# Performance work log

Measured on AMD Instinct MI355X. Metric: run time of the kernel, lower is better.

## Reference

```python
import jax, jax.numpy as jnp
import numpy as np

K = 32          # num_sets (experts)
D_IN = 10       # input_size
D_H = 20        # hidden_size
D_OUT = 1       # output_size
B = 262144      # batch


def setup_inputs() -> dict:
    key = jax.random.key(0)
    ks = jax.random.split(key, 6)
    # Kaiming-uniform-ish init scale like torch Linear defaults
    s1 = 1.0 / np.sqrt(D_IN)
    s2 = 1.0 / np.sqrt(D_H)
    return {
        "input_data": jax.random.normal(ks[0], (B, D_IN), dtype=jnp.float32),
        "W1": jax.random.uniform(ks[1], (K, D_H, D_IN), jnp.float32, -s1, s1),
        "b1": jax.random.uniform(ks[2], (K, D_H), jnp.float32, -s1, s1),
        "W2": jax.random.uniform(ks[3], (K, D_OUT, D_H), jnp.float32, -s2, s2),
        "b2": jax.random.uniform(ks[4], (K, D_OUT), jnp.float32, -s2, s2),
        "prototypes": jax.random.normal(ks[5], (K, D_IN), dtype=jnp.float32),
    }


def reference(input_data, W1, b1, W2, b2, prototypes):
    # All K tiny experts as one batched GEMM: [B,K,H]
    h = jax.nn.relu(jnp.einsum("bi,khi->bkh", input_data, W1) + b1[None])
    preds = jnp.einsum("bkh,koh->bko", h, W2) + b2[None]          # [B,K,O]
    # Distance-based softmax gating over experts
    diff = input_data[:, None, :] - prototypes[None, :, :]        # [B,K,D]
    dist = jnp.sqrt(jnp.sum(diff * diff, axis=2))                 # [B,K]
    attn = jax.nn.softmax(-dist, axis=1)                          # [B,K]
    return jnp.sum(preds * attn[:, :, None], axis=1)              # [B,O]
```

## Files before the change

### kernel.cpp

```cpp
#include <hip/hip_runtime.h>


#define KX 32
#define DIN 10
#define DH 20
#define BLOCK 512
#define WPB 8
#define TPW 2

typedef short bf16x8 __attribute__((ext_vector_type(8)));
typedef float f32x16 __attribute__((ext_vector_type(16)));
typedef float v2f    __attribute__((ext_vector_type(2)));

#define ZERO16 {0.f,0.f,0.f,0.f, 0.f,0.f,0.f,0.f, 0.f,0.f,0.f,0.f, 0.f,0.f,0.f,0.f}

__device__ inline unsigned short f2bf(float f) {
    unsigned int u = __float_as_uint(f);
    unsigned int r = u + 0x7fffu + ((u >> 16) & 1u);
    return (unsigned short)(r >> 16);
}

union BFU { bf16x8 v; unsigned short s[8]; };

__global__ __launch_bounds__(BLOCK, 4) void moe_kernel(
    const float* __restrict__ x,
    const float* __restrict__ W1,
    const float* __restrict__ b1,
    const float* __restrict__ W2,
    const float* __restrict__ b2,
    const float* __restrict__ proto,
    float* __restrict__ out,
    int B)
{
    __shared__ bf16x8 s_af[KX * 40];
    __shared__ float  s_w2[KX * 24];
    __shared__ bf16x8 s_pf[64];
    __shared__ float  s_pn2[32];
    __shared__ float  s_b2c[32];

    const int tid = threadIdx.x;

    for (int idx = tid; idx < KX * 40; idx += BLOCK) {
        const int e = idx / 40, rem = idx - e * 40;
        const int ks = rem / 20, h = rem - ks * 20;
        BFU u;
#pragma unroll
        for (int j = 0; j < 8; ++j) {
            const int kk = ks * 8 + j;
            float v = 0.f;
            if (kk < DIN) v = W1[(e * DH + h) * DIN + kk];
            else if (kk == DIN) v = b1[e * DH + h];
            u.s[j] = f2bf(v);
        }
        s_af[idx] = u.v;
    }
    for (int idx = tid; idx < KX * 24; idx += BLOCK) {
        const int e = idx / 24, rem = idx - e * 24;
        const int hf = rem / 12, q = rem - hf * 12;
        float v = 0.f;
        if (q < 10) {
            const int m = (q & 3) + 8 * (q >> 2) + 4 * hf;
            const int h = (m & 3) + 4 * (m >> 3) + ((m & 4) ? 10 : 0);
            v = W2[e * DH + h];
        }
        s_w2[idx] = v;
    }
    if (tid < 64) {
        const int m = tid & 31, kb = (tid >> 5) * 8;
        BFU u;
#pragma unroll
        for (int j = 0; j < 8; ++j) {
            const int kk = kb + j;
            u.s[j] = f2bf(kk < DIN ? proto[m * DIN + kk] : 0.f);
        }
        s_pf[tid] = u.v;
    }
    if (tid < 32) {
        const int hf = tid >> 4, q = tid & 15;
        const int p = (q & 3) + 8 * (q >> 2) + 4 * hf;
        float s = 0.f;
#pragma unroll
        for (int i = 0; i < DIN; ++i) { const float v = proto[p * DIN + i]; s = fmaf(v, v, s); }
        s_pn2[tid] = s;
        s_b2c[tid] = b2[p];
    }
    __syncthreads();

    const int lane = tid & 63;
    const int wave = tid >> 6;
    const int half = lane >> 5;
    const int col  = lane & 31;
    const bf16x8 pfrag = s_pf[lane];

    const f32x16 kZero = ZERO16;

    const int m = col;
    const bool mvalid = (m & 4) ? (m < 22) : (m < 18);
    const int hidx = (m & 3) + 4 * (m >> 3) + ((m & 4) ? 10 : 0);
    const int abase = half * 20 + (mvalid ? hidx : 0);

#pragma unroll 1
    for (int t = 0; t < TPW; ++t) {
        const int row = ((blockIdx.x * WPB + wave) * TPW + t) * 32 + col;
        const int rr = (row < B) ? row : (B - 1);

        float xe[8];
        const float* xr = x + (size_t)rr * DIN;
        if (half == 0) {
#pragma unroll
            for (int i = 0; i < 4; ++i) {
                const float2 v = *(const float2*)(xr + 2 * i);
                xe[2 * i] = v.x; xe[2 * i + 1] = v.y;
            }
        } else {
            const float2 v = *(const float2*)(xr + 8);
            xe[0] = v.x; xe[1] = v.y; xe[2] = 1.f;
            xe[3] = 0.f; xe[4] = 0.f; xe[5] = 0.f; xe[6] = 0.f; xe[7] = 0.f;
        }
        BFU xu;
#pragma unroll
        for (int j = 0; j < 8; ++j) xu.s[j] = f2bf(xe[j]);
        const bf16x8 xfrag = xu.v;

        float part;
        if (half == 0) {
            part = 0.f;
#pragma unroll
            for (int j = 0; j < 8; ++j) part = fmaf(xe[j], xe[j], part);
        } else {
            part = fmaf(xe[0], xe[0], xe[1] * xe[1]);
        }
        const float xn2 = part + __shfl_xor(part, 32);

        const f32x16 dotg = __builtin_amdgcn_mfma_f32_32x32x16_bf16(pfrag, xfrag, kZero, 0, 0, 0);

        float gate[16], gx[16];
        float dsum = 0.f;
        float nsA = 0.f, nsB = 0.f;
        {
            const float* pn2h = s_pn2 + half * 16;
            const float* b2c  = s_b2c + half * 16;
#pragma unroll
            for (int q = 0; q < 16; ++q) {
                float d2 = fmaf(dotg[q], -2.f, xn2 + pn2h[q]);
                d2 = fmaxf(d2, 0.f);
                const float g = __expf(-__fsqrt_rn(d2));
                gate[q] = g;
                dsum += g;
                nsA = fmaf(g, b2c[q], nsA);
            }
#pragma unroll
            for (int q = 0; q < 16; ++q) gx[q] = __shfl_xor(gate[q], 32);
        }

#pragma unroll 2
        for (int j = 0; j < 16; ++j) {
            const int elo = (j & 3) + 8 * (j >> 2);
            const int ehi = elo + 4;

            bf16x8 alo = {0, 0, 0, 0, 0, 0, 0, 0};
            bf16x8 ahi = {0, 0, 0, 0, 0, 0, 0, 0};
            if (mvalid) {
                alo = s_af[elo * 40 + abase];
                ahi = s_af[ehi * 40 + abase];
            }
            const f32x16 clo = __builtin_amdgcn_mfma_f32_32x32x16_bf16(alo, xfrag, kZero, 0, 0, 0);
            const f32x16 chi = __builtin_amdgcn_mfma_f32_32x32x16_bf16(ahi, xfrag, kZero, 0, 0, 0);

            const float4* w4lo = (const float4*)(s_w2 + elo * 24 + half * 12);
            const float4* w4hi = (const float4*)(s_w2 + ehi * 24 + half * 12);
            v2f plov = v2f{0.f, 0.f}, phiv = v2f{0.f, 0.f};
#pragma unroll
            for (int i = 0; i < 3; ++i) {
                const float4 wl = w4lo[i];
                const float4 wh = w4hi[i];
                v2f cl0 = __builtin_elementwise_max(v2f{clo[4 * i + 0], clo[4 * i + 1]}, v2f{0.f, 0.f});
                v2f cl1 = __builtin_elementwise_max(v2f{clo[4 * i + 2], clo[4 * i + 3]}, v2f{0.f, 0.f});
                v2f ch0 = __builtin_elementwise_max(v2f{chi[4 * i + 0], chi[4 * i + 1]}, v2f{0.f, 0.f});
                v2f ch1 = __builtin_elementwise_max(v2f{chi[4 * i + 2], chi[4 * i + 3]}, v2f{0.f, 0.f});
                plov = __builtin_elementwise_fma(cl0, v2f{wl.x, wl.y}, plov);
                plov = __builtin_elementwise_fma(cl1, v2f{wl.z, wl.w}, plov);
                phiv = __builtin_elementwise_fma(ch0, v2f{wh.x, wh.y}, phiv);
                phiv = __builtin_elementwise_fma(ch1, v2f{wh.z, wh.w}, phiv);
            }
            const float pplo = plov.x + plov.y;
            const float pphi = phiv.x + phiv.y;

            const float p_own = half ? pphi : pplo;
            const float p_oth = half ? pplo : pphi;
            nsA = fmaf(gate[j], p_own, nsA);
            nsB = fmaf(gx[j],   p_oth, nsB);
        }

        float nsum = nsA + nsB;
        nsum += __shfl_xor(nsum, 32);
        dsum += __shfl_xor(dsum, 32);
        if (half == 0 && row < B) out[row] = nsum / dsum;
    }
}

extern "C" void kernel_launch(void* const* d_in, const int* in_sizes, int n_in,
                              void* d_out, int out_size, void* d_ws, size_t ws_size,
                              hipStream_t stream) {
    const float* x     = (const float*)d_in[0];
    const float* W1    = (const float*)d_in[1];
    const float* b1    = (const float*)d_in[2];
    const float* W2    = (const float*)d_in[3];
    const float* b2    = (const float*)d_in[4];
    const float* proto = (const float*)d_in[5];
    float* out = (float*)d_out;

    const int B = out_size;
    const int rows_per_block = WPB * TPW * 32;
    const int grid = (B + rows_per_block - 1) / rows_per_block;
    hipLaunchKernelGGL(moe_kernel, dim3(grid), dim3(BLOCK), 0, stream,
                       x, W1, b1, W2, b2, proto, out, B);
}
```

Baseline: 96.74 us.

## Interchange tile and expert loops to reuse W1/W2 fragments across row tiles

The loop order changes so both row tiles per wave are processed inside the expert loop. Each expert's A-fragment and W2 LDS reads are now loaded once and reused for both tiles, which cuts LDS traffic. The gate shuffle is replaced by shuffling the partial predictions, and b2 is read straight from global memory instead of staged through shared memory. The cost is higher register pressure from holding the gates for both tiles, plus more cross-lane shuffles per expert.

```diff
diff --git a/kernel.cpp b/kernel.cpp
--- a/kernel.cpp
+++ b/kernel.cpp
@@ -36,7 +36,6 @@
     __shared__ float  s_w2[KX * 24];
     __shared__ bf16x8 s_pf[64];
     __shared__ float  s_pn2[32];
-    __shared__ float  s_b2c[32];
 
     const int tid = threadIdx.x;
 
@@ -82,7 +81,6 @@
 #pragma unroll
         for (int i = 0; i < DIN; ++i) { const float v = proto[p * DIN + i]; s = fmaf(v, v, s); }
         s_pn2[tid] = s;
-        s_b2c[tid] = b2[p];
     }
     __syncthreads();
 
@@ -91,7 +89,6 @@
     const int half = lane >> 5;
     const int col  = lane & 31;
     const bf16x8 pfrag = s_pf[lane];
-
     const f32x16 kZero = ZERO16;
 
     const int m = col;
@@ -99,10 +96,15 @@
     const int hidx = (m & 3) + 4 * (m >> 3) + ((m & 4) ? 10 : 0);
     const int abase = half * 20 + (mvalid ? hidx : 0);
 
-#pragma unroll 1
+    int   row[TPW];
+    bf16x8 xfrag[TPW];
+    float gate[TPW][16];
+    float nsum[TPW], dsum[TPW];
+
+#pragma unroll
     for (int t = 0; t < TPW; ++t) {
-        const int row = ((blockIdx.x * WPB + wave) * TPW + t) * 32 + col;
-        const int rr = (row < B) ? row : (B - 1);
+        row[t] = ((blockIdx.x * WPB + wave) * TPW + t) * 32 + col;
+        const int rr = (row[t] < B) ? row[t] : (B - 1);
 
         float xe[8];
         const float* xr = x + (size_t)rr * DIN;
@@ -120,7 +122,7 @@
         BFU xu;
 #pragma unroll
         for (int j = 0; j < 8; ++j) xu.s[j] = f2bf(xe[j]);
-        const bf16x8 xfrag = xu.v;
+        xfrag[t] = xu.v;
 
         float part;
         if (half == 0) {
@@ -132,70 +134,85 @@
         }
         const float xn2 = part + __shfl_xor(part, 32);
 
-        const f32x16 dotg = __builtin_amdgcn_mfma_f32_32x32x16_bf16(pfrag, xfrag, kZero, 0, 0, 0);
-
-        float gate[16], gx[16];
-        float dsum = 0.f;
-        float nsA = 0.f, nsB = 0.f;
-        {
-            const float* pn2h = s_pn2 + half * 16;
-            const float* b2c  = s_b2c + half * 16;
-#pragma unroll
-            for (int q = 0; q < 16; ++q) {
-                float d2 = fmaf(dotg[q], -2.f, xn2 + pn2h[q]);
-                d2 = fmaxf(d2, 0.f);
-                const float g = __expf(-__fsqrt_rn(d2));
-                gate[q] = g;
-                dsum += g;
-                nsA = fmaf(g, b2c[q], nsA);
-            }
-#pragma unroll
-            for (int q = 0; q < 16; ++q) gx[q] = __shfl_xor(gate[q], 32);
-        }
+        const f32x16 dotg = __builtin_amdgcn_mfma_f32_32x32x16_bf16(pfrag, xfrag[t], kZero, 0, 0, 0);
+        const float* pn2h = s_pn2 + half * 16;
+        float ds = 0.f;
+#pragma unroll
+        for (int q = 0; q < 16; ++q) {
+            float d2 = fmaf(dotg[q], -2.f, xn2 + pn2h[q]);
+            d2 = fmaxf(d2, 0.f);
+            const float g = __expf(-__fsqrt_rn(d2));
+            gate[t][q] = g;
+            ds += g;
+        }
+        dsum[t] = ds;
+        nsum[t] = 0.f;
+    }
 
 #pragma unroll 2
-        for (int j = 0; j < 16; ++j) {
-            const int elo = (j & 3) + 8 * (j >> 2);
-            const int ehi = elo + 4;
-
-            bf16x8 alo = {0, 0, 0, 0, 0, 0, 0, 0};
-            bf16x8 ahi = {0, 0, 0, 0, 0, 0, 0, 0};
-            if (mvalid) {
-                alo = s_af[elo * 40 + abase];
-                ahi = s_af[ehi * 40 + abase];
-            }
-            const f32x16 clo = __builtin_amdgcn_mfma_f32_32x32x16_bf16(alo, xfrag, kZero, 0, 0, 0);
-            const f32x16 chi = __builtin_amdgcn_mfma_f32_32x32x16_bf16(ahi, xfrag, kZero, 0, 0, 0);
-
-            const float4* w4lo = (const float4*)(s_w2 + elo * 24 + half * 12);
-            const float4* w4hi = (const float4*)(s_w2 + ehi * 24 + half * 12);
+    for (int j = 0; j < 16; ++j) {
+        const int elo = (j & 3) + 8 * (j >> 2);
+        const int ehi = elo + 4;
+
+        bf16x8 alo = {0, 0, 0, 0, 0, 0, 0, 0};
+        bf16x8 ahi = {0, 0, 0, 0, 0, 0, 0, 0};
+        if (mvalid) {
+            alo = s_af[elo * 40 + abase];
+            ahi = s_af[ehi * 40 + abase];
+        }
+        const float4* w4lo = (const float4*)(s_w2 + elo * 24 + half * 12);
+        const float4* w4hi = (const float4*)(s_w2 + ehi * 24 + half * 12);
+        const float4 wl0 = w4lo[0], wl1 = w4lo[1], wl2 = w4lo[2];
+        const float4 wh0 = w4hi[0], wh1 = w4hi[1], wh2 = w4hi[2];
+
+#pragma unroll
+        for (int t = 0; t < TPW; ++t) {
+            const f32x16 clo = __builtin_amdgcn_mfma_f32_32x32x16_bf16(alo, xfrag[t], kZero, 0, 0, 0);
+            const f32x16 chi = __builtin_amdgcn_mfma_f32_32x32x16_bf16(ahi, xfrag[t], kZero, 0, 0, 0);
+
             v2f plov = v2f{0.f, 0.f}, phiv = v2f{0.f, 0.f};
-#pragma unroll
-            for (int i = 0; i < 3; ++i) {
-                const float4 wl = w4lo[i];
-                const float4 wh = w4hi[i];
-                v2f cl0 = __builtin_elementwise_max(v2f{clo[4 * i + 0], clo[4 * i + 1]}, v2f{0.f, 0.f});
-                v2f cl1 = __builtin_elementwise_max(v2f{clo[4 * i + 2], clo[4 * i + 3]}, v2f{0.f, 0.f});
-                v2f ch0 = __builtin_elementwise_max(v2f{chi[4 * i + 0], chi[4 * i + 1]}, v2f{0.f, 0.f});
-                v2f ch1 = __builtin_elementwise_max(v2f{chi[4 * i + 2], chi[4 * i + 3]}, v2f{0.f, 0.f});
-                plov = __builtin_elementwise_fma(cl0, v2f{wl.x, wl.y}, plov);
-                plov = __builtin_elementwise_fma(cl1, v2f{wl.z, wl.w}, plov);
-                phiv = __builtin_elementwise_fma(ch0, v2f{wh.x, wh.y}, phiv);
-                phiv = __builtin_elementwise_fma(ch1, v2f{wh.z, wh.w}, phiv);
+            {
+                v2f c;
+                c = __builtin_elementwise_max(v2f{clo[0],  clo[1]},  v2f{0.f, 0.f});
+                plov = __builtin_elementwise_fma(c, v2f{wl0.x, wl0.y}, plov);
+                c = __builtin_elementwise_max(v2f{clo[2],  clo[3]},  v2f{0.f, 0.f});
+                plov = __builtin_elementwise_fma(c, v2f{wl0.z, wl0.w}, plov);
+                c = __builtin_elementwise_max(v2f{clo[4],  clo[5]},  v2f{0.f, 0.f});
+                plov = __builtin_elementwise_fma(c, v2f{wl1.x, wl1.y}, plov);
+                c = __builtin_elementwise_max(v2f{clo[6],  clo[7]},  v2f{0.f, 0.f});
+                plov = __builtin_elementwise_fma(c, v2f{wl1.z, wl1.w}, plov);
+                c = __builtin_elementwise_max(v2f{clo[8],  clo[9]},  v2f{0.f, 0.f});
+                plov = __builtin_elementwise_fma(c, v2f{wl2.x, wl2.y}, plov);
+                c = __builtin_elementwise_max(v2f{clo[10], clo[11]}, v2f{0.f, 0.f});
+                plov = __builtin_elementwise_fma(c, v2f{wl2.z, wl2.w}, plov);
+
+                c = __builtin_elementwise_max(v2f{chi[0],  chi[1]},  v2f{0.f, 0.f});
+                phiv = __builtin_elementwise_fma(c, v2f{wh0.x, wh0.y}, phiv);
+                c = __builtin_elementwise_max(v2f{chi[2],  chi[3]},  v2f{0.f, 0.f});
+                phiv = __builtin_elementwise_fma(c, v2f{wh0.z, wh0.w}, phiv);
+                c = __builtin_elementwise_max(v2f{chi[4],  chi[5]},  v2f{0.f, 0.f});
+                phiv = __builtin_elementwise_fma(c, v2f{wh1.x, wh1.y}, phiv);
+                c = __builtin_elementwise_max(v2f{chi[6],  chi[7]},  v2f{0.f, 0.f});
+                phiv = __builtin_elementwise_fma(c, v2f{wh1.z, wh1.w}, phiv);
+                c = __builtin_elementwise_max(v2f{chi[8],  chi[9]},  v2f{0.f, 0.f});
+                phiv = __builtin_elementwise_fma(c, v2f{wh2.x, wh2.y}, phiv);
+                c = __builtin_elementwise_max(v2f{chi[10], chi[11]}, v2f{0.f, 0.f});
+                phiv = __builtin_elementwise_fma(c, v2f{wh2.z, wh2.w}, phiv);
             }
             const float pplo = plov.x + plov.y;
             const float pphi = phiv.x + phiv.y;
-
-            const float p_own = half ? pphi : pplo;
-            const float p_oth = half ? pplo : pphi;
-            nsA = fmaf(gate[j], p_own, nsA);
-            nsB = fmaf(gx[j],   p_oth, nsB);
-        }
-
-        float nsum = nsA + nsB;
-        nsum += __shfl_xor(nsum, 32);
-        dsum += __shfl_xor(dsum, 32);
-        if (half == 0 && row < B) out[row] = nsum / dsum;
+            const float plo = pplo + __shfl_xor(pplo, 32);
+            const float phi = pphi + __shfl_xor(pphi, 32);
+            const float pred = half ? (phi + b2[ehi]) : (plo + b2[elo]);
+            nsum[t] = fmaf(gate[t][j], pred, nsum[t]);
+        }
+    }
+
+#pragma unroll
+    for (int t = 0; t < TPW; ++t) {
+        float ns = nsum[t] + __shfl_xor(nsum[t], 32);
+        float ds = dsum[t] + __shfl_xor(dsum[t], 32);
+        if (half == 0 && row[t] < B) out[row[t]] = ns / ds;
     }
 }
 
```

Result: no change. 94.91 us (-1.9%).
